# Optimization experiments

Measured on AMD Instinct MI355X. Metric: run time of the kernel, lower is better.

The kernel has to match this reference:

```python
import jax, jax.numpy as jnp
import numpy as np

N, E, G, S = 200000, 800000, 2048, 128
NUM_OPS, NUM_ETYPES, NUMERIC = 64, 4, 12
H, TEXT, VOCAB, OUT = 256, 64, 30000, 512
IN0 = 32 + NUMERIC  # 44


def _ln(h, eps=1e-5):
    # nn.LayerNorm with default (ones/zeros) affine, created fresh each forward
    m = h.mean(-1, keepdims=True)
    v = ((h - m) ** 2).mean(-1, keepdims=True)
    return (h - m) * jax.lax.rsqrt(v + eps)


def _leaky(v):
    return jnp.where(v > 0, v, 0.1 * v)  # LeakyReLU(0.1)


def setup_inputs() -> dict:
    key = jax.random.key(0)
    ks = jax.random.split(key, 40)
    x = jax.random.normal(ks[0], (N, 1 + NUMERIC), jnp.float32)
    x = x.at[:, 0].set(jax.random.randint(ks[1], (N,), 0, NUM_OPS).astype(jnp.float32))
    inp = {
        'x': x,
        'edge_index': jax.random.randint(ks[2], (2, E), 0, N),
        'edge_attr': jax.random.randint(ks[3], (E,), 0, NUM_ETYPES),
        'batch': jnp.sort(jax.random.randint(ks[4], (N,), 0, G)),
        'sql_ids': jax.random.randint(ks[5], (G, S), 0, VOCAB),
        'sql_mask': (jax.random.uniform(ks[6], (G, S)) > 0.3).astype(jnp.float32),
        'op_embed': jax.random.normal(ks[7], (NUM_OPS, 32), jnp.float32),
        'edge_embed': jax.random.normal(ks[8], (NUM_ETYPES, 16), jnp.float32),
        'token_embed': jax.random.normal(ks[9], (VOCAB, TEXT), jnp.float32).at[0].set(0.0),  # padding_idx=0
    }
    dims = [IN0, H, H]
    k = 10
    for i, d in enumerate(dims):
        inp[f'lin_w{i}'] = jax.random.normal(ks[k], (d, 16), jnp.float32) * 0.05; k += 1
        inp[f'lin_b{i}'] = jnp.zeros((d,), jnp.float32)
        inp[f'eps{i}'] = jnp.zeros((), jnp.float32)  # train_eps init 0
        inp[f'W1_{i}'] = jax.random.normal(ks[k], (H, d), jnp.float32) * 0.05; k += 1
        inp[f'b1_{i}'] = jnp.zeros((H,), jnp.float32)
        inp[f'W2_{i}'] = jax.random.normal(ks[k], (H, H), jnp.float32) * 0.05; k += 1
        inp[f'b2_{i}'] = jnp.zeros((H,), jnp.float32)
    inp['mW1'] = jax.random.normal(ks[k], (H, H + 3 + TEXT), jnp.float32) * 0.05; k += 1
    inp['mb1'] = jnp.zeros((H,), jnp.float32)
    inp['mW2'] = jax.random.normal(ks[k], (OUT, H), jnp.float32) * 0.05
    inp['mb2'] = jnp.zeros((OUT,), jnp.float32)
    return inp


def reference(x, edge_index, edge_attr, batch, sql_ids, sql_mask,
              op_embed, edge_embed, token_embed,
              lin_w0, lin_b0, eps0, W1_0, b1_0, W2_0, b2_0,
              lin_w1, lin_b1, eps1, W1_1, b1_1, W2_1, b2_1,
              lin_w2, lin_b2, eps2, W1_2, b1_2, W2_2, b2_2,
              mW1, mb1, mW2, mb2):
    op_ids = jnp.clip(x[:, 0].astype(jnp.int32), 0, NUM_OPS - 1)
    nums = x[:, 1:]
    e_idx = jnp.minimum(edge_attr, NUM_ETYPES - 1)  # clamp_max
    edge_emb = edge_embed[e_idx]                    # [E,16]
    h = jnp.concatenate([op_embed[op_ids], nums], 1)  # [N,44]
    src, dst = edge_index[0], edge_index[1]
    convs = [(lin_w0, lin_b0, eps0, W1_0, b1_0, W2_0, b2_0),
             (lin_w1, lin_b1, eps1, W1_1, b1_1, W2_1, b2_1),
             (lin_w2, lin_b2, eps2, W1_2, b1_2, W2_2, b2_2)]
    for (lw, lb, eps, W1, b1, W2, b2) in convs:
        h_in = h
        # GINEConv: msg = relu(x_j + Lin(edge_attr)); sum-aggregate at dst
        msg = jax.nn.relu(h[src] + edge_emb @ lw.T + lb)        # [E,d]
        aggr = jax.ops.segment_sum(msg, dst, num_segments=h.shape[0])
        z = (1.0 + eps) * h + aggr
        h = jax.nn.relu(z @ W1.T + b1) @ W2.T + b2              # conv MLP -> [N,H]
        h = _ln(h)
        h = _leaky(h + h_in) if h_in.shape[-1] == h.shape[-1] else _leaky(h)
    # graph pooling
    g = jax.ops.segment_sum(h, batch, num_segments=G)            # global_add_pool
    count = jax.ops.segment_sum(jnp.ones((h.shape[0],), h.dtype), batch, num_segments=G)
    denom = jnp.maximum(count, 1.0)                              # scatter_mean semantics
    fanout_mean = jax.ops.segment_sum(x[:, 5], batch, num_segments=G) / denom
    cost_mean = jax.ops.segment_sum(x[:, 4], batch, num_segments=G) / denom
    graph_sum = jnp.stack([count, fanout_mean, cost_mean], 1)    # [G,3]
    # text pooling (masked mean)
    emb = token_embed[sql_ids]                                   # [G,S,TEXT]
    summed = (emb * sql_mask[..., None]).sum(1)
    lengths = jnp.maximum(sql_mask.sum(1, keepdims=True), 1.0)
    text_feat = summed / lengths
    cat = jnp.concatenate([g, graph_sum, text_feat], 1)          # [G, H+3+TEXT]
    hid = _leaky(cat @ mW1.T + mb1)                              # Dropout(0.1) is identity in eval
    return hid @ mW2.T + mb2                                     # [G, OUT]
```

## Files before the change

kernel.cpp:

```cpp
#include <hip/hip_runtime.h>

#define NN 200000
#define EE 800000
#define GG 2048
#define NBLK ((NN + 255) / 256)

typedef __attribute__((ext_vector_type(8))) short short8;
typedef __attribute__((ext_vector_type(4))) float f32x4;

__device__ __forceinline__ float bf2f(ushort u){
  unsigned x = ((unsigned)u) << 16;
  return __uint_as_float(x);
}
__device__ __forceinline__ ushort f2bf(float f){
  unsigned x = __float_as_uint(f);
  x += 0x7fffu + ((x >> 16) & 1u);
  return (ushort)(x >> 16);
}

__device__ __forceinline__ void swz256(const float* __restrict__ W, ushort* __restrict__ o, int idx){
  int ks = idx >> 13, rem = idx & 8191;
  int j16 = rem >> 9, rem2 = rem & 511;
  int ln = rem2 >> 3, t = rem2 & 7;
  int row = j16*16 + (ln & 15);
  int k = ks*32 + (ln >> 4)*8 + t;
  o[idx] = f2bf(W[(size_t)row*256 + k]);
}

__global__ __launch_bounds__(256) void prep_k(
    const float* __restrict__ W10, const float* __restrict__ W20,
    const float* __restrict__ W11, const float* __restrict__ W21,
    const float* __restrict__ W12, const float* __restrict__ W22,
    const float* __restrict__ lw0, const float* __restrict__ lb0,
    const float* __restrict__ lw1, const float* __restrict__ lb1,
    const float* __restrict__ lw2, const float* __restrict__ lb2,
    const float* __restrict__ eE, const float* __restrict__ mW1,
    const float* __restrict__ mW2,
    ushort* __restrict__ wb10, ushort* __restrict__ wb20,
    ushort* __restrict__ wb11, ushort* __restrict__ wb21,
    ushort* __restrict__ wb12, ushort* __restrict__ wb22,
    ushort* __restrict__ mW1b, ushort* __restrict__ mW2b,
    float* __restrict__ eb)
{
  int b = blockIdx.x, tid = threadIdx.x;
  if (b < 64){
    int idx = b*256 + tid;
    int ks = idx >> 13, rem = idx & 8191;
    int j16 = rem >> 9, rem2 = rem & 511;
    int ln = rem2 >> 3, t = rem2 & 7;
    int row = j16*16 + (ln & 15);
    int k = ks*32 + (ln >> 4)*8 + t;
    wb10[idx] = (k < 44) ? f2bf(W10[row*44 + k]) : (ushort)0;
    return;
  }
  b -= 64;
  if (b < 256){ swz256(W20, wb20, b*256+tid); return; } b -= 256;
  if (b < 256){ swz256(W11, wb11, b*256+tid); return; } b -= 256;
  if (b < 256){ swz256(W21, wb21, b*256+tid); return; } b -= 256;
  if (b < 256){ swz256(W12, wb12, b*256+tid); return; } b -= 256;
  if (b < 256){ swz256(W22, wb22, b*256+tid); return; } b -= 256;
  if (b < 384){
    int idx = b*256 + tid; int o = idx / 384, k = idx - o*384;
    mW1b[idx] = (k < 323) ? f2bf(mW1[(size_t)o*323 + k]) : (ushort)0;
    return;
  }
  b -= 384;
  if (b < 512){ int idx = b*256+tid; mW2b[idx] = f2bf(mW2[idx]); return; } b -= 512;
  int li = b >> 2, t = b & 3;
  const float* lw = (li == 0) ? lw0 : ((li == 1) ? lw1 : lw2);
  const float* lb = (li == 0) ? lb0 : ((li == 1) ? lb1 : lb2);
  int d = (li == 0) ? 44 : 256;
  float v = 0.f;
  if (tid < d){
    float a = 0.f;
    #pragma unroll
    for (int j = 0; j < 16; j++) a += eE[t*16 + j] * lw[tid*16 + j];
    v = a + lb[tid];
  }
  eb[(li*4 + t)*256 + tid] = v;
}

__global__ __launch_bounds__(256) void build_h0_k(
    const float* __restrict__ x, const float* __restrict__ opE, ushort* __restrict__ h0)
{
  int idx = blockIdx.x*256 + threadIdx.x;
  int i = idx >> 6, c = idx & 63;
  float v = 0.f;
  if (c < 32){
    int op = (int)x[(size_t)i*13];
    op = op < 0 ? 0 : (op > 63 ? 63 : op);
    v = opE[op*32 + c];
  } else if (c < 44){
    v = x[(size_t)i*13 + (c - 31)];
  }
  h0[idx] = f2bf(v);
}

__global__ __launch_bounds__(256) void deg_k(const int* __restrict__ dst, int* __restrict__ D){
  int e = blockIdx.x*256 + threadIdx.x;
  atomicAdd(&D[dst[e]], 1);
}
__global__ __launch_bounds__(256) void scan1_k(int* __restrict__ D, int* __restrict__ bsum){
  __shared__ int s[256];
  int b = blockIdx.x, t = threadIdx.x, idx = b*256 + t;
  int v = (idx < NN) ? D[idx] : 0;
  s[t] = v; __syncthreads();
  for (int off = 1; off < 256; off <<= 1){
    int u = (t >= off) ? s[t-off] : 0;
    __syncthreads();
    s[t] += u;
    __syncthreads();
  }
  if (idx < NN) D[idx] = s[t] - v;
  if (t == 255) bsum[b] = s[255];
}
__global__ __launch_bounds__(256) void scan2_k(int* __restrict__ bsum){
  __shared__ int s[256];
  __shared__ int carry;
  int t = threadIdx.x;
  if (t == 0) carry = 0;
  __syncthreads();
  for (int c0 = 0; c0 < NBLK; c0 += 256){
    int idx = c0 + t;
    int v = (idx < NBLK) ? bsum[idx] : 0;
    s[t] = v; __syncthreads();
    for (int off = 1; off < 256; off <<= 1){
      int u = (t >= off) ? s[t-off] : 0;
      __syncthreads();
      s[t] += u;
      __syncthreads();
    }
    int ex = s[t] - v + carry;
    if (idx < NBLK) bsum[idx] = ex;
    int tot = s[255];
    __syncthreads();
    if (t == 0) carry += tot;
    __syncthreads();
  }
}
__global__ __launch_bounds__(256) void scan3_k(int* __restrict__ D, const int* __restrict__ bsum){
  int b = blockIdx.x, idx = b*256 + threadIdx.x;
  if (idx < NN) D[idx] += bsum[b];
}
__global__ __launch_bounds__(256) void fill_k(const int* __restrict__ src, const int* __restrict__ dst,
                                              const int* __restrict__ et, int* __restrict__ D,
                                              int* __restrict__ csr){
  int e = blockIdx.x*256 + threadIdx.x;
  int d = dst[e];
  int t = et[e]; t = t < 3 ? t : 3;
  int pos = atomicAdd(&D[d], 1);
  csr[pos] = src[e] | (t << 18);
}

template<int KD, int RESID>
__global__ __launch_bounds__(256) void layerf_k(
    const ushort* __restrict__ hsrc, const int* __restrict__ Dend, const int* __restrict__ csr,
    const float* __restrict__ ebL,
    const ushort* __restrict__ W1s, const float* __restrict__ b1,
    const ushort* __restrict__ W2s, const float* __restrict__ b2,
    const float* __restrict__ epsp, ushort* __restrict__ hout)
{
  __shared__ ushort ZT[32][264];
  __shared__ ushort HT[RESID ? 32 : 1][264];
  __shared__ float ebs[1024];
  __shared__ float red1[32][4], red2[32][4], mnL[32], rsL[32];
  const int tid = threadIdx.x, lane = tid & 63, wv = tid >> 6;
  const int l15 = lane & 15, lq = lane >> 4;
  const int rowBase = blockIdx.x * 32;
  const float epv = 1.0f + epsp[0];
  const char* hb = (const char*)hsrc;

  if (KD == 256){
    for (int i = tid; i < 1024; i += 256) ebs[i] = ebL[i];
  } else {
    if (tid < 256) ebs[tid] = ebL[(tid >> 6)*256 + (tid & 63)];
  }
  __syncthreads();

  if (KD == 256){
    int nz; asm("v_mov_b32 %0, 0" : "=v"(nz));
    const int c = lane * 4;
    const unsigned c2 = lane * 8;
    #pragma unroll 1
    for (int it = 0; it < 2; it++){
      int rr0 = wv*8 + it*4;
      int r0 = rowBase + rr0;
      float4 A0, A1, A2, A3;
      {
        ushort4 q0 = *(const ushort4*)(hb + (size_t)(r0+0)*512 + c2);
        ushort4 q1 = *(const ushort4*)(hb + (size_t)(r0+1)*512 + c2);
        ushort4 q2 = *(const ushort4*)(hb + (size_t)(r0+2)*512 + c2);
        ushort4 q3 = *(const ushort4*)(hb + (size_t)(r0+3)*512 + c2);
        if (RESID){
          *(ushort4*)&HT[rr0+0][c] = q0;
          *(ushort4*)&HT[rr0+1][c] = q1;
          *(ushort4*)&HT[rr0+2][c] = q2;
          *(ushort4*)&HT[rr0+3][c] = q3;
        }
        A0 = make_float4(epv*bf2f(q0.x), epv*bf2f(q0.y), epv*bf2f(q0.z), epv*bf2f(q0.w));
        A1 = make_float4(epv*bf2f(q1.x), epv*bf2f(q1.y), epv*bf2f(q1.z), epv*bf2f(q1.w));
        A2 = make_float4(epv*bf2f(q2.x), epv*bf2f(q2.y), epv*bf2f(q2.z), epv*bf2f(q2.w));
        A3 = make_float4(epv*bf2f(q3.x), epv*bf2f(q3.y), epv*bf2f(q3.z), epv*bf2f(q3.w));
      }
      int bm1 = (r0 == 0) ? 0 : Dend[r0-1];
      int e0 = Dend[r0], e1 = Dend[r0+1], e2 = Dend[r0+2], e3 = Dend[r0+3];
      int st0 = bm1, st1 = e0, st2 = e1, st3 = e2;
      int n0 = e0 - st0, n1 = e1 - st1, n2 = e2 - st2, n3 = e3 - st3;
      int nmax = n0 > n1 ? n0 : n1;
      nmax = nmax > n2 ? nmax : n2;
      nmax = nmax > n3 ? nmax : n3;
      ushort4 z4; z4.x = z4.y = z4.z = z4.w = 0;
      ushort4 sv0 = z4, sv1 = z4, sv2 = z4, sv3 = z4;
      int t0 = 0, t1 = 0, t2 = 0, t3 = 0;
      int q0 = 0, q1 = 0, q2 = 0, q3 = 0;
      if (n0 > 0){ int p = csr[st0 + nz]; sv0 = *(const ushort4*)(hb + (unsigned)((p & 0x3FFFF) << 9) + c2); t0 = ((p >> 18) & 3)*256; }
      if (n1 > 0){ int p = csr[st1 + nz]; sv1 = *(const ushort4*)(hb + (unsigned)((p & 0x3FFFF) << 9) + c2); t1 = ((p >> 18) & 3)*256; }
      if (n2 > 0){ int p = csr[st2 + nz]; sv2 = *(const ushort4*)(hb + (unsigned)((p & 0x3FFFF) << 9) + c2); t2 = ((p >> 18) & 3)*256; }
      if (n3 > 0){ int p = csr[st3 + nz]; sv3 = *(const ushort4*)(hb + (unsigned)((p & 0x3FFFF) << 9) + c2); t3 = ((p >> 18) & 3)*256; }
      if (n0 > 1) q0 = csr[st0 + 1 + nz];
      if (n1 > 1) q1 = csr[st1 + 1 + nz];
      if (n2 > 1) q2 = csr[st2 + 1 + nz];
      if (n3 > 1) q3 = csr[st3 + 1 + nz];
      for (int k = 0; k < nmax; k++){
        ushort4 c0 = sv0, c1 = sv1, c2v = sv2, c3 = sv3;
        int u0 = t0, u1 = t1, u2 = t2, u3 = t3;
        if (k+1 < n0){ int p = q0; sv0 = *(const ushort4*)(hb + (unsigned)((p & 0x3FFFF) << 9) + c2); t0 = ((p >> 18) & 3)*256; if (k+2 < n0) q0 = csr[st0 + k + 2 + nz]; }
        if (k+1 < n1){ int p = q1; sv1 = *(const ushort4*)(hb + (unsigned)((p & 0x3FFFF) << 9) + c2); t1 = ((p >> 18) & 3)*256; if (k+2 < n1) q1 = csr[st1 + k + 2 + nz]; }
        if (k+1 < n2){ int p = q2; sv2 = *(const ushort4*)(hb + (unsigned)((p & 0x3FFFF) << 9) + c2); t2 = ((p >> 18) & 3)*256; if (k+2 < n2) q2 = csr[st2 + k + 2 + nz]; }
        if (k+1 < n3){ int p = q3; sv3 = *(const ushort4*)(hb + (unsigned)((p & 0x3FFFF) << 9) + c2); t3 = ((p >> 18) & 3)*256; if (k+2 < n3) q3 = csr[st3 + k + 2 + nz]; }
        if (k < n0){
          const float4 ev = *(const float4*)&ebs[u0 + c];
          float v;
          v = bf2f(c0.x) + ev.x; A0.x += v > 0.f ? v : 0.f;
          v = bf2f(c0.y) + ev.y; A0.y += v > 0.f ? v : 0.f;
          v = bf2f(c0.z) + ev.z; A0.z += v > 0.f ? v : 0.f;
          v = bf2f(c0.w) + ev.w; A0.w += v > 0.f ? v : 0.f;
        }
        if (k < n1){
          const float4 ev = *(const float4*)&ebs[u1 + c];
          float v;
          v = bf2f(c1.x) + ev.x; A1.x += v > 0.f ? v : 0.f;
          v = bf2f(c1.y) + ev.y; A1.y += v > 0.f ? v : 0.f;
          v = bf2f(c1.z) + ev.z; A1.z += v > 0.f ? v : 0.f;
          v = bf2f(c1.w) + ev.w; A1.w += v > 0.f ? v : 0.f;
        }
        if (k < n2){
          const float4 ev = *(const float4*)&ebs[u2 + c];
          float v;
          v = bf2f(c2v.x) + ev.x; A2.x += v > 0.f ? v : 0.f;
          v = bf2f(c2v.y) + ev.y; A2.y += v > 0.f ? v : 0.f;
          v = bf2f(c2v.z) + ev.z; A2.z += v > 0.f ? v : 0.f;
          v = bf2f(c2v.w) + ev.w; A2.w += v > 0.f ? v : 0.f;
        }
        if (k < n3){
          const float4 ev = *(const float4*)&ebs[u3 + c];
          float v;
          v = bf2f(c3.x) + ev.x; A3.x += v > 0.f ? v : 0.f;
          v = bf2f(c3.y) + ev.y; A3.y += v > 0.f ? v : 0.f;
          v = bf2f(c3.z) + ev.z; A3.z += v > 0.f ? v : 0.f;
          v = bf2f(c3.w) + ev.w; A3.w += v > 0.f ? v : 0.f;
        }
      }
      ushort4 o;
      o.x = f2bf(A0.x); o.y = f2bf(A0.y); o.z = f2bf(A0.z); o.w = f2bf(A0.w);
      *(ushort4*)&ZT[rr0+0][c] = o;
      o.x = f2bf(A1.x); o.y = f2bf(A1.y); o.z = f2bf(A1.z); o.w = f2bf(A1.w);
      *(ushort4*)&ZT[rr0+1][c] = o;
      o.x = f2bf(A2.x); o.y = f2bf(A2.y); o.z = f2bf(A2.z); o.w = f2bf(A2.w);
      *(ushort4*)&ZT[rr0+2][c] = o;
      o.x = f2bf(A3.x); o.y = f2bf(A3.y); o.z = f2bf(A3.z); o.w = f2bf(A3.w);
      *(ushort4*)&ZT[rr0+3][c] = o;
    }
  } else {
    const int c = l15 * 4;
    const unsigned c2 = l15 * 8;
    const int rrA = wv*8 + lq, rrB = rrA + 4;
    const int rA = rowBase + rrA, rB = rowBase + rrB;
    float aA0, aA1, aA2, aA3, aB0, aB1, aB2, aB3;
    {
      ushort4 hv = *(const ushort4*)(hb + (size_t)rA*128 + c2);
      aA0 = epv*bf2f(hv.x); aA1 = epv*bf2f(hv.y); aA2 = epv*bf2f(hv.z); aA3 = epv*bf2f(hv.w);
      hv = *(const ushort4*)(hb + (size_t)rB*128 + c2);
      aB0 = epv*bf2f(hv.x); aB1 = epv*bf2f(hv.y); aB2 = epv*bf2f(hv.z); aB3 = epv*bf2f(hv.w);
    }
    int stA = (rA == 0) ? 0 : Dend[rA-1], enA = Dend[rA];
    int stB = Dend[rB-1], enB = Dend[rB];
    int nA = enA - stA, nB = enB - stB;
    int nmax = nA > nB ? nA : nB;
    ushort4 svA, svB; int ttA = 0, ttB = 0, pA = 0, pB = 0;
    svA.x = svA.y = svA.z = svA.w = 0; svB = svA;
    if (nA > 0){ int p = csr[stA]; svA = *(const ushort4*)(hb + (unsigned)((p & 0x3FFFF) << 7) + c2); ttA = ((p >> 18) & 3)*64; }
    if (nB > 0){ int p = csr[stB]; svB = *(const ushort4*)(hb + (unsigned)((p & 0x3FFFF) << 7) + c2); ttB = ((p >> 18) & 3)*64; }
    if (nA > 1) pA = csr[stA+1];
    if (nB > 1) pB = csr[stB+1];
    for (int k = 0; k < nmax; k++){
      if (k < nA){
        ushort4 cu = svA;
        const float4 ev = *(const float4*)&ebs[ttA + c];
        if (k+1 < nA){
          int p = pA;
          svA = *(const ushort4*)(hb + (unsigned)((p & 0x3FFFF) << 7) + c2);
          ttA = ((p >> 18) & 3)*64;
          if (k+2 < nA) pA = csr[stA+k+2];
        }
        float v;
        v = bf2f(cu.x) + ev.x; aA0 += v > 0.f ? v : 0.f;
        v = bf2f(cu.y) + ev.y; aA1 += v > 0.f ? v : 0.f;
        v = bf2f(cu.z) + ev.z; aA2 += v > 0.f ? v : 0.f;
        v = bf2f(cu.w) + ev.w; aA3 += v > 0.f ? v : 0.f;
      }
      if (k < nB){
        ushort4 cu = svB;
        const float4 ev = *(const float4*)&ebs[ttB + c];
        if (k+1 < nB){
          int p = pB;
          svB = *(const ushort4*)(hb + (unsigned)((p & 0x3FFFF) << 7) + c2);
          ttB = ((p >> 18) & 3)*64;
          if (k+2 < nB) pB = csr[stB+k+2];
        }
        float v;
        v = bf2f(cu.x) + ev.x; aB0 += v > 0.f ? v : 0.f;
        v = bf2f(cu.y) + ev.y; aB1 += v > 0.f ? v : 0.f;
        v = bf2f(cu.z) + ev.z; aB2 += v > 0.f ? v : 0.f;
        v = bf2f(cu.w) + ev.w; aB3 += v > 0.f ? v : 0.f;
      }
    }
    ushort4 o;
    o.x = f2bf(aA0); o.y = f2bf(aA1); o.z = f2bf(aA2); o.w = f2bf(aA3);
    *(ushort4*)&ZT[rrA][c] = o;
    o.x = f2bf(aB0); o.y = f2bf(aB1); o.z = f2bf(aB2); o.w = f2bf(aB3);
    *(ushort4*)&ZT[rrB][c] = o;
  }
  __syncthreads();

  f32x4 acc[2][4];
  #pragma unroll
  for (int i = 0; i < 2; i++)
    #pragma unroll
    for (int j = 0; j < 4; j++){ f32x4 z = {0.f,0.f,0.f,0.f}; acc[i][j] = z; }

  #pragma unroll
  for (int s = 0; s < KD/32; s++){
    short8 af[2], bfv[4];
    #pragma unroll
    for (int j = 0; j < 4; j++)
      bfv[j] = *(const short8*)(W1s + ((size_t)(s*16 + wv*4 + j)*64 + lane)*8);
    #pragma unroll
    for (int i = 0; i < 2; i++)
      af[i] = *(const short8*)&ZT[i*16 + l15][s*32 + lq*8];
    #pragma unroll
    for (int i = 0; i < 2; i++)
      #pragma unroll
      for (int j = 0; j < 4; j++)
        acc[i][j] = __builtin_amdgcn_mfma_f32_16x16x32_bf16(af[i], bfv[j], acc[i][j], 0, 0, 0);
  }
  __syncthreads();

  {
    float b1c[4];
    #pragma unroll
    for (int j = 0; j < 4; j++) b1c[j] = b1[wv*64 + j*16 + l15];
    #pragma unroll
    for (int i = 0; i < 2; i++)
      #pragma unroll
      for (int j = 0; j < 4; j++){
        int cc = wv*64 + j*16 + l15;
        #pragma unroll
        for (int rg = 0; rg < 4; rg++){
          int r = i*16 + (lq << 2) + rg;
          float v = acc[i][j][rg] + b1c[j];
          v = v > 0.f ? v : 0.f;
          ZT[r][cc] = f2bf(v);
        }
      }
  }
  __syncthreads();

  #pragma unroll
  for (int i = 0; i < 2; i++)
    #pragma unroll
    for (int j = 0; j < 4; j++){ f32x4 z = {0.f,0.f,0.f,0.f}; acc[i][j] = z; }

  #pragma unroll
  for (int s = 0; s < 8; s++){
    short8 af[2], bfv[4];
    #pragma unroll
    for (int j = 0; j < 4; j++)
      bfv[j] = *(const short8*)(W2s + ((size_t)(s*16 + wv*4 + j)*64 + lane)*8);
    #pragma unroll
    for (int i = 0; i < 2; i++)
      af[i] = *(const short8*)&ZT[i*16 + l15][s*32 + lq*8];
    #pragma unroll
    for (int i = 0; i < 2; i++)
      #pragma unroll
      for (int j = 0; j < 4; j++)
        acc[i][j] = __builtin_amdgcn_mfma_f32_16x16x32_bf16(af[i], bfv[j], acc[i][j], 0, 0, 0);
  }

  float b2c[4];
  #pragma unroll
  for (int j = 0; j < 4; j++) b2c[j] = b2[wv*64 + j*16 + l15];
  #pragma unroll
  for (int i = 0; i < 2; i++){
    #pragma unroll
    for (int rg = 0; rg < 4; rg++){
      float s1 = 0.f, s2 = 0.f;
      #pragma unroll
      for (int j = 0; j < 4; j++){
        float y = acc[i][j][rg] + b2c[j];
        s1 += y; s2 += y*y;
      }
      #pragma unroll
      for (int m = 1; m < 16; m <<= 1){
        s1 += __shfl_xor(s1, m, 64);
        s2 += __shfl_xor(s2, m, 64);
      }
      if (l15 == 0){
        int r = i*16 + (lq << 2) + rg;
        red1[r][wv] = s1; red2[r][wv] = s2;
      }
    }
  }
  __syncthreads();
  if (tid < 32){
    float s1 = red1[tid][0] + red1[tid][1] + red1[tid][2] + red1[tid][3];
    float s2 = red2[tid][0] + red2[tid][1] + red2[tid][2] + red2[tid][3];
    float mn = s1 * (1.f/256.f);
    float vr = s2 * (1.f/256.f) - mn*mn;
    mnL[tid] = mn;
    rsL[tid] = rsqrtf(vr + 1e-5f);
  }
  __syncthreads();
  #pragma unroll
  for (int i = 0; i < 2; i++){
    #pragma unroll
    for (int rg = 0; rg < 4; rg++){
      int r = i*16 + (lq << 2) + rg;
      float mn = mnL[r], rs = rsL[r];
      #pragma unroll
      for (int j = 0; j < 4; j++){
        int cc = wv*64 + j*16 + l15;
        float y = acc[i][j][rg] + b2c[j];
        float v = (y - mn) * rs;
        if (!RESID) v = v > 0.f ? v : 0.1f*v;
        ZT[r][cc] = f2bf(v);
      }
    }
  }
  __syncthreads();
  #pragma unroll
  for (int p = 0; p < 8; p++){
    int r = p*4 + (tid >> 6);
    int cs = (tid & 63) * 4;
    ushort4 zt = *(const ushort4*)&ZT[r][cs];
    ushort4 o;
    if (RESID){
      ushort4 rv = *(const ushort4*)&HT[r][cs];
      float v0 = bf2f(zt.x) + bf2f(rv.x);
      float v1 = bf2f(zt.y) + bf2f(rv.y);
      float v2 = bf2f(zt.z) + bf2f(rv.z);
      float v3 = bf2f(zt.w) + bf2f(rv.w);
      o.x = f2bf(v0 > 0.f ? v0 : 0.1f*v0);
      o.y = f2bf(v1 > 0.f ? v1 : 0.1f*v1);
      o.z = f2bf(v2 > 0.f ? v2 : 0.1f*v2);
      o.w = f2bf(v3 > 0.f ? v3 : 0.1f*v3);
    } else {
      o = zt;
    }
    *(ushort4*)(hout + (size_t)(rowBase + r)*256 + cs) = o;
  }
}

__global__ __launch_bounds__(256) void readout_k(
    const ushort* __restrict__ h, const int* __restrict__ batch, const float* __restrict__ x,
    const int* __restrict__ sqlIds, const float* __restrict__ sqlMask,
    const float* __restrict__ tok, ushort* __restrict__ catb)
{
  int g = blockIdx.x, tid = threadIdx.x;
  const int lane = tid & 63, wv = tid >> 6;
  __shared__ int se[2];
  __shared__ float part[4][256];
  __shared__ float tpart[4][64];
  __shared__ float mpart[4];
  __shared__ float xs[2];
  if (tid < 2){
    int target = g + tid;
    int lo = 0, hi = NN;
    while (lo < hi){ int mid = (lo + hi) >> 1; if (batch[mid] < target) lo = mid + 1; else hi = mid; }
    se[tid] = lo;
  }
  __syncthreads();
  int start = se[0], end = se[1];
  {
    float a0 = 0.f, a1 = 0.f, a2 = 0.f, a3 = 0.f;
    for (int i = start + wv; i < end; i += 4){
      ushort4 q = *(const ushort4*)(h + (size_t)i*256 + lane*4);
      a0 += bf2f(q.x); a1 += bf2f(q.y); a2 += bf2f(q.z); a3 += bf2f(q.w);
    }
    part[wv][lane*4 + 0] = a0;
    part[wv][lane*4 + 1] = a1;
    part[wv][lane*4 + 2] = a2;
    part[wv][lane*4 + 3] = a3;
  }
  if (wv >= 2){
    int col = (wv == 2) ? 5 : 4;
    float s = 0.f;
    for (int i = start + lane; i < end; i += 64) s += x[(size_t)i*13 + col];
    #pragma unroll
    for (int m = 1; m < 64; m <<= 1) s += __shfl_xor(s, m, 64);
    if (lane == 0) xs[wv - 2] = s;
  }
  {
    int c = lane;
    float acc = 0.f, m = 0.f;
    for (int s = wv; s < 128; s += 4){
      int id = sqlIds[g*128 + s];
      float mk = sqlMask[g*128 + s];
      m += mk;
      acc += tok[(size_t)id*64 + c] * mk;
    }
    tpart[wv][c] = acc;
    if (c == 0) mpart[wv] = m;
  }
  __syncthreads();
  {
    float gsum = part[0][tid] + part[1][tid] + part[2][tid] + part[3][tid];
    catb[(size_t)g*384 + tid] = f2bf(gsum);
  }
  if (tid == 0){
    float cnt = (float)(end - start);
    float dn = cnt > 1.f ? cnt : 1.f;
    catb[(size_t)g*384 + 256] = f2bf(cnt);
    catb[(size_t)g*384 + 257] = f2bf(xs[0] / dn);
    catb[(size_t)g*384 + 258] = f2bf(xs[1] / dn);
  }
  if (tid < 64){
    float L = mpart[0] + mpart[1] + mpart[2] + mpart[3];
    L = L > 1.f ? L : 1.f;
    float tsum = tpart[0][tid] + tpart[1][tid] + tpart[2][tid] + tpart[3][tid];
    catb[(size_t)g*384 + 259 + tid] = f2bf(tsum / L);
  }
  if (tid >= 64 && tid < 125){
    catb[(size_t)g*384 + 259 + tid] = 0;
  }
}

__global__ __launch_bounds__(256) void head1_k(
    const ushort* __restrict__ catb, const ushort* __restrict__ W1b,
    const float* __restrict__ b1, ushort* __restrict__ hidb)
{
  __shared__ ushort smem[64*72 + 256*72];
  ushort (*As)[72] = (ushort(*)[72])smem;
  ushort (*Ws)[72] = (ushort(*)[72])(smem + 64*72);
  const int tid = threadIdx.x, lane = tid & 63, wv = tid >> 6;
  const int rowBase = blockIdx.x * 64;
  f32x4 acc[4][4];
  #pragma unroll
  for (int i = 0; i < 4; i++)
    #pragma unroll
    for (int j = 0; j < 4; j++){ f32x4 z = {0.f,0.f,0.f,0.f}; acc[i][j] = z; }

  for (int k0 = 0; k0 < 384; k0 += 64){
    __syncthreads();
    #pragma unroll
    for (int p = 0; p < 4; p++){
      int r = p*16 + (tid >> 4);
      int kk = (tid & 15) * 4;
      *(ushort4*)&As[r][kk] = *(const ushort4*)(catb + (size_t)(rowBase + r)*384 + k0 + kk);
    }
    #pragma unroll
    for (int p = 0; p < 16; p++){
      int oc = p*16 + (tid >> 4);
      int kk = (tid & 15) * 4;
      *(ushort4*)&Ws[oc][kk] = *(const ushort4*)(W1b + (size_t)oc*384 + k0 + kk);
    }
    __syncthreads();
    #pragma unroll
    for (int kc = 0; kc < 2; kc++){
      short8 af[4], bfv[4];
      #pragma unroll
      for (int i = 0; i < 4; i++)
        af[i] = *(const short8*)&As[i*16 + (lane & 15)][kc*32 + (lane >> 4)*8];
      #pragma unroll
      for (int j = 0; j < 4; j++)
        bfv[j] = *(const short8*)&Ws[wv*64 + j*16 + (lane & 15)][kc*32 + (lane >> 4)*8];
      #pragma unroll
      for (int i = 0; i < 4; i++)
        #pragma unroll
        for (int j = 0; j < 4; j++)
          acc[i][j] = __builtin_amdgcn_mfma_f32_16x16x32_bf16(af[i], bfv[j], acc[i][j], 0, 0, 0);
    }
  }
  __syncthreads();
  ushort (*Cs)[264] = (ushort(*)[264])smem;
  #pragma unroll
  for (int j = 0; j < 4; j++){
    int cc = wv*64 + j*16 + (lane & 15);
    float bb = b1[cc];
    #pragma unroll
    for (int i = 0; i < 4; i++){
      #pragma unroll
      for (int rg = 0; rg < 4; rg++){
        int r = i*16 + ((lane >> 4) << 2) + rg;
        float v = acc[i][j][rg] + bb;
        v = v > 0.f ? v : 0.1f*v;
        Cs[r][cc] = f2bf(v);
      }
    }
  }
  __syncthreads();
  #pragma unroll
  for (int p = 0; p < 16; p++){
    int r = p*4 + (tid >> 6);
    int c = (tid & 63) * 4;
    *(ushort4*)(hidb + (size_t)(rowBase + r)*256 + c) = *(const ushort4*)&Cs[r][c];
  }
}

__global__ __launch_bounds__(256) void head2_k(
    const ushort* __restrict__ hidb, const ushort* __restrict__ W2b,
    const float* __restrict__ b2, float* __restrict__ out)
{
  __shared__ float smemf[128*132];
  ushort (*As)[72] = (ushort(*)[72])smemf;
  ushort (*Bs)[72] = (ushort(*)[72])((ushort*)smemf + 128*72);
  const int tid = threadIdx.x, lane = tid & 63, wv = tid >> 6;
  const int wr = (wv >> 1) * 64;
  const int wc = (wv & 1) * 64;
  const int rowBase = blockIdx.x * 128;
  const int colBase = blockIdx.y * 128;
  const int lr = tid >> 4, lk = (tid & 15) * 4;

  f32x4 acc[4][4];
  #pragma unroll
  for (int i = 0; i < 4; i++)
    #pragma unroll
    for (int j = 0; j < 4; j++){ f32x4 z = {0.f,0.f,0.f,0.f}; acc[i][j] = z; }

  for (int k0 = 0; k0 < 256; k0 += 64){
    __syncthreads();
    #pragma unroll
    for (int p = 0; p < 8; p++){
      int r = lr + p*16;
      *(ushort4*)&As[r][lk] = *(const ushort4*)(hidb + (size_t)(rowBase + r)*256 + k0 + lk);
      *(ushort4*)&Bs[r][lk] = *(const ushort4*)(W2b + (size_t)(colBase + r)*256 + k0 + lk);
    }
    __syncthreads();
    #pragma unroll
    for (int kc = 0; kc < 2; kc++){
      short8 af[4], bfv[4];
      #pragma unroll
      for (int i = 0; i < 4; i++)
        af[i] = *(const short8*)&As[wr + i*16 + (lane & 15)][kc*32 + (lane >> 4)*8];
      #pragma unroll
      for (int j = 0; j < 4; j++)
        bfv[j] = *(const short8*)&Bs[wc + j*16 + (lane & 15)][kc*32 + (lane >> 4)*8];
      #pragma unroll
      for (int i = 0; i < 4; i++)
        #pragma unroll
        for (int j = 0; j < 4; j++)
          acc[i][j] = __builtin_amdgcn_mfma_f32_16x16x32_bf16(af[i], bfv[j], acc[i][j], 0, 0, 0);
    }
  }
  __syncthreads();
  float (*Cs)[132] = (float(*)[132])smemf;
  #pragma unroll
  for (int j = 0; j < 4; j++){
    int cl = wc + j*16 + (lane & 15);
    float bb = b2[colBase + cl];
    #pragma unroll
    for (int i = 0; i < 4; i++){
      int r0 = wr + i*16 + ((lane >> 4) << 2);
      #pragma unroll
      for (int rg = 0; rg < 4; rg++)
        Cs[r0 + rg][cl] = acc[i][j][rg] + bb;
    }
  }
  __syncthreads();
  #pragma unroll
  for (int p = 0; p < 16; p++){
    int r = (tid >> 5) + p*8;
    int c4 = (tid & 31) * 4;
    *(float4*)(out + (size_t)(rowBase + r)*512 + colBase + c4) = *(const float4*)&Cs[r][c4];
  }
}

extern "C" void kernel_launch(void* const* d_in, const int* in_sizes, int n_in,
                              void* d_out, int out_size, void* d_ws, size_t ws_size,
                              hipStream_t stream)
{
  const float* x       = (const float*)d_in[0];
  const int*   ei      = (const int*)d_in[1];
  const int*   src     = ei;
  const int*   dst     = ei + EE;
  const int*   eattr   = (const int*)d_in[2];
  const int*   batch   = (const int*)d_in[3];
  const int*   sqlIds  = (const int*)d_in[4];
  const float* sqlMask = (const float*)d_in[5];
  const float* opE     = (const float*)d_in[6];
  const float* eE      = (const float*)d_in[7];
  const float* tok     = (const float*)d_in[8];
  const float* lw0 = (const float*)d_in[9],  *lb0 = (const float*)d_in[10], *eps0 = (const float*)d_in[11];
  const float* W10 = (const float*)d_in[12], *b10 = (const float*)d_in[13];
  const float* W20 = (const float*)d_in[14], *b20 = (const float*)d_in[15];
  const float* lw1 = (const float*)d_in[16], *lb1 = (const float*)d_in[17], *eps1 = (const float*)d_in[18];
  const float* W11 = (const float*)d_in[19], *b11 = (const float*)d_in[20];
  const float* W21 = (const float*)d_in[21], *b21 = (const float*)d_in[22];
  const float* lw2 = (const float*)d_in[23], *lb2 = (const float*)d_in[24], *eps2 = (const float*)d_in[25];
  const float* W12 = (const float*)d_in[26], *b12 = (const float*)d_in[27];
  const float* W22 = (const float*)d_in[28], *b22 = (const float*)d_in[29];
  const float* mW1 = (const float*)d_in[30], *mb1 = (const float*)d_in[31];
  const float* mW2 = (const float*)d_in[32], *mb2 = (const float*)d_in[33];
  float* out = (float*)d_out;

  char* ws = (char*)d_ws;
  size_t off = 0;
  const size_t NB256 = (size_t)NN*256*2;
  ushort* bufH    = (ushort*)(ws + off); off += NB256;
  char*   region  = ws + off;            off += NB256;
  ushort* h0      = (ushort*)region;
  ushort* hPong   = (ushort*)region;
  ushort* catb    = (ushort*)region;
  ushort* hidb    = (ushort*)(region + (size_t)GG*384*2);
  ushort* wb10 = (ushort*)(ws + off); off += (size_t)256*64*2;
  ushort* wb20 = (ushort*)(ws + off); off += (size_t)65536*2;
  ushort* wb11 = (ushort*)(ws + off); off += (size_t)65536*2;
  ushort* wb21 = (ushort*)(ws + off); off += (size_t)65536*2;
  ushort* wb12 = (ushort*)(ws + off); off += (size_t)65536*2;
  ushort* wb22 = (ushort*)(ws + off); off += (size_t)65536*2;
  ushort* mW1b = (ushort*)(ws + off); off += (size_t)256*384*2;
  ushort* mW2b = (ushort*)(ws + off); off += (size_t)512*256*2;
  float*  eb   = (float*)(ws + off);  off += (size_t)3*4*256*4;
  int* D    = (int*)(ws + off); off += (size_t)NN*4;
  int* bsum = (int*)(ws + off); off += (size_t)NBLK*4;
  int* csr  = (int*)(ws + off); off += (size_t)EE*4;
  size_t needFast = off;

  if (ws_size < needFast) return;

  prep_k<<<2252, 256, 0, stream>>>(W10, W20, W11, W21, W12, W22,
                                   lw0, lb0, lw1, lb1, lw2, lb2, eE, mW1, mW2,
                                   wb10, wb20, wb11, wb21, wb12, wb22, mW1b, mW2b, eb);
  build_h0_k<<<50000, 256, 0, stream>>>(x, opE, h0);

  hipMemsetAsync(D, 0, (size_t)NN*4, stream);
  deg_k<<<3125, 256, 0, stream>>>(dst, D);
  scan1_k<<<NBLK, 256, 0, stream>>>(D, bsum);
  scan2_k<<<1, 256, 0, stream>>>(bsum);
  scan3_k<<<NBLK, 256, 0, stream>>>(D, bsum);
  fill_k<<<3125, 256, 0, stream>>>(src, dst, eattr, D, csr);

  layerf_k<64,0><<<6250, 256, 0, stream>>>(h0,    D, csr, eb,        wb10, b10, wb20, b20, eps0, bufH);
  layerf_k<256,1><<<6250, 256, 0, stream>>>(bufH, D, csr, eb + 1024, wb11, b11, wb21, b21, eps1, hPong);
  layerf_k<256,1><<<6250, 256, 0, stream>>>(hPong,D, csr, eb + 2048, wb12, b12, wb22, b22, eps2, bufH);

  readout_k<<<GG, 256, 0, stream>>>(bufH, batch, x, sqlIds, sqlMask, tok, catb);
  head1_k<<<32, 256, 0, stream>>>(catb, mW1b, mb1, hidb);
  head2_k<<<dim3(16, 4), 256, 0, stream>>>(hidb, mW2b, mb2, out);
}
```

Measured before the change: 832.8 us.

## Gather neighbor features from int8 per-row-quantized shadow copies in GIN layers

Layers 0 and 1 now also write an 8-bit per-row-scaled copy of their output plus a per-row scale. Layers 1 and 2 read that int8 copy in the edge-gather aggregation instead of bf16 rows, which halves the bytes fetched per neighbor. The bf16 output is still written for the residual path and readout. The shadow path runs only when the workspace is large enough. This adds extra writes, a wave-wide max reduction per row and quantization error in the aggregation.

```diff
diff --git a/kernel.cpp b/kernel.cpp
--- a/kernel.cpp
+++ b/kernel.cpp
@@ -152,13 +152,15 @@
   csr[pos] = src[e] | (t << 18);
 }
 
-template<int KD, int RESID>
+template<int KD, int RESID, int WRS, int RDS>
 __global__ __launch_bounds__(256) void layerf_k(
     const ushort* __restrict__ hsrc, const int* __restrict__ Dend, const int* __restrict__ csr,
     const float* __restrict__ ebL,
     const ushort* __restrict__ W1s, const float* __restrict__ b1,
     const ushort* __restrict__ W2s, const float* __restrict__ b2,
-    const float* __restrict__ epsp, ushort* __restrict__ hout)
+    const float* __restrict__ epsp, ushort* __restrict__ hout,
+    const unsigned char* __restrict__ q8in, const float* __restrict__ sclin,
+    unsigned char* __restrict__ q8out, float* __restrict__ sclout)
 {
   __shared__ ushort ZT[32][264];
   __shared__ ushort HT[RESID ? 32 : 1][264];
@@ -181,6 +183,7 @@
     int nz; asm("v_mov_b32 %0, 0" : "=v"(nz));
     const int c = lane * 4;
     const unsigned c2 = lane * 8;
+    const unsigned c1 = lane * 4;
     #pragma unroll 1
     for (int it = 0; it < 2; it++){
       int rr0 = wv*8 + it*4;
@@ -209,56 +212,113 @@
       int nmax = n0 > n1 ? n0 : n1;
       nmax = nmax > n2 ? nmax : n2;
       nmax = nmax > n3 ? nmax : n3;
-      ushort4 z4; z4.x = z4.y = z4.z = z4.w = 0;
-      ushort4 sv0 = z4, sv1 = z4, sv2 = z4, sv3 = z4;
-      int t0 = 0, t1 = 0, t2 = 0, t3 = 0;
-      int q0 = 0, q1 = 0, q2 = 0, q3 = 0;
-      if (n0 > 0){ int p = csr[st0 + nz]; sv0 = *(const ushort4*)(hb + (unsigned)((p & 0x3FFFF) << 9) + c2); t0 = ((p >> 18) & 3)*256; }
-      if (n1 > 0){ int p = csr[st1 + nz]; sv1 = *(const ushort4*)(hb + (unsigned)((p & 0x3FFFF) << 9) + c2); t1 = ((p >> 18) & 3)*256; }
-      if (n2 > 0){ int p = csr[st2 + nz]; sv2 = *(const ushort4*)(hb + (unsigned)((p & 0x3FFFF) << 9) + c2); t2 = ((p >> 18) & 3)*256; }
-      if (n3 > 0){ int p = csr[st3 + nz]; sv3 = *(const ushort4*)(hb + (unsigned)((p & 0x3FFFF) << 9) + c2); t3 = ((p >> 18) & 3)*256; }
-      if (n0 > 1) q0 = csr[st0 + 1 + nz];
-      if (n1 > 1) q1 = csr[st1 + 1 + nz];
-      if (n2 > 1) q2 = csr[st2 + 1 + nz];
-      if (n3 > 1) q3 = csr[st3 + 1 + nz];
-      for (int k = 0; k < nmax; k++){
-        ushort4 c0 = sv0, c1 = sv1, c2v = sv2, c3 = sv3;
-        int u0 = t0, u1 = t1, u2 = t2, u3 = t3;
-        if (k+1 < n0){ int p = q0; sv0 = *(const ushort4*)(hb + (unsigned)((p & 0x3FFFF) << 9) + c2); t0 = ((p >> 18) & 3)*256; if (k+2 < n0) q0 = csr[st0 + k + 2 + nz]; }
-        if (k+1 < n1){ int p = q1; sv1 = *(const ushort4*)(hb + (unsigned)((p & 0x3FFFF) << 9) + c2); t1 = ((p >> 18) & 3)*256; if (k+2 < n1) q1 = csr[st1 + k + 2 + nz]; }
-        if (k+1 < n2){ int p = q2; sv2 = *(const ushort4*)(hb + (unsigned)((p & 0x3FFFF) << 9) + c2); t2 = ((p >> 18) & 3)*256; if (k+2 < n2) q2 = csr[st2 + k + 2 + nz]; }
-        if (k+1 < n3){ int p = q3; sv3 = *(const ushort4*)(hb + (unsigned)((p & 0x3FFFF) << 9) + c2); t3 = ((p >> 18) & 3)*256; if (k+2 < n3) q3 = csr[st3 + k + 2 + nz]; }
-        if (k < n0){
-          const float4 ev = *(const float4*)&ebs[u0 + c];
-          float v;
-          v = bf2f(c0.x) + ev.x; A0.x += v > 0.f ? v : 0.f;
-          v = bf2f(c0.y) + ev.y; A0.y += v > 0.f ? v : 0.f;
-          v = bf2f(c0.z) + ev.z; A0.z += v > 0.f ? v : 0.f;
-          v = bf2f(c0.w) + ev.w; A0.w += v > 0.f ? v : 0.f;
+
+      if (RDS){
+        unsigned sv0 = 0, sv1 = 0, sv2 = 0, sv3 = 0;
+        float ss0 = 0.f, ss1 = 0.f, ss2 = 0.f, ss3 = 0.f;
+        int t0 = 0, t1 = 0, t2 = 0, t3 = 0;
+        int q0 = 0, q1 = 0, q2 = 0, q3 = 0;
+        if (n0 > 0){ int p = csr[st0 + nz]; unsigned rw = (unsigned)(p & 0x3FFFF); sv0 = *(const unsigned*)(q8in + ((size_t)rw<<8) + c1); ss0 = sclin[rw]; t0 = ((p >> 18) & 3)*256; }
+        if (n1 > 0){ int p = csr[st1 + nz]; unsigned rw = (unsigned)(p & 0x3FFFF); sv1 = *(const unsigned*)(q8in + ((size_t)rw<<8) + c1); ss1 = sclin[rw]; t1 = ((p >> 18) & 3)*256; }
+        if (n2 > 0){ int p = csr[st2 + nz]; unsigned rw = (unsigned)(p & 0x3FFFF); sv2 = *(const unsigned*)(q8in + ((size_t)rw<<8) + c1); ss2 = sclin[rw]; t2 = ((p >> 18) & 3)*256; }
+        if (n3 > 0){ int p = csr[st3 + nz]; unsigned rw = (unsigned)(p & 0x3FFFF); sv3 = *(const unsigned*)(q8in + ((size_t)rw<<8) + c1); ss3 = sclin[rw]; t3 = ((p >> 18) & 3)*256; }
+        if (n0 > 1) q0 = csr[st0 + 1 + nz];
+        if (n1 > 1) q1 = csr[st1 + 1 + nz];
+        if (n2 > 1) q2 = csr[st2 + 1 + nz];
+        if (n3 > 1) q3 = csr[st3 + 1 + nz];
+        for (int k = 0; k < nmax; k++){
+          unsigned c0 = sv0, c1v = sv1, c2v = sv2, c3v = sv3;
+          float d0 = ss0, d1 = ss1, d2 = ss2, d3 = ss3;
+          int u0 = t0, u1 = t1, u2 = t2, u3 = t3;
+          if (k+1 < n0){ int p = q0; unsigned rw = (unsigned)(p & 0x3FFFF); sv0 = *(const unsigned*)(q8in + ((size_t)rw<<8) + c1); ss0 = sclin[rw]; t0 = ((p >> 18) & 3)*256; if (k+2 < n0) q0 = csr[st0 + k + 2 + nz]; }
+          if (k+1 < n1){ int p = q1; unsigned rw = (unsigned)(p & 0x3FFFF); sv1 = *(const unsigned*)(q8in + ((size_t)rw<<8) + c1); ss1 = sclin[rw]; t1 = ((p >> 18) & 3)*256; if (k+2 < n1) q1 = csr[st1 + k + 2 + nz]; }
+          if (k+1 < n2){ int p = q2; unsigned rw = (unsigned)(p & 0x3FFFF); sv2 = *(const unsigned*)(q8in + ((size_t)rw<<8) + c1); ss2 = sclin[rw]; t2 = ((p >> 18) & 3)*256; if (k+2 < n2) q2 = csr[st2 + k + 2 + nz]; }
+          if (k+1 < n3){ int p = q3; unsigned rw = (unsigned)(p & 0x3FFFF); sv3 = *(const unsigned*)(q8in + ((size_t)rw<<8) + c1); ss3 = sclin[rw]; t3 = ((p >> 18) & 3)*256; if (k+2 < n3) q3 = csr[st3 + k + 2 + nz]; }
+          if (k < n0){
+            const float4 ev = *(const float4*)&ebs[u0 + c];
+            float o = d0 * -128.f, v;
+            v = fmaf((float)(c0 & 0xffu),        d0, o) + ev.x; A0.x += v > 0.f ? v : 0.f;
+            v = fmaf((float)((c0 >> 8) & 0xffu), d0, o) + ev.y; A0.y += v > 0.f ? v : 0.f;
+            v = fmaf((float)((c0 >> 16) & 0xffu),d0, o) + ev.z; A0.z += v > 0.f ? v : 0.f;
+            v = fmaf((float)(c0 >> 24),          d0, o) + ev.w; A0.w += v > 0.f ? v : 0.f;
+          }
+          if (k < n1){
+            const float4 ev = *(const float4*)&ebs[u1 + c];
+            float o = d1 * -128.f, v;
+            v = fmaf((float)(c1v & 0xffu),        d1, o) + ev.x; A1.x += v > 0.f ? v : 0.f;
+            v = fmaf((float)((c1v >> 8) & 0xffu), d1, o) + ev.y; A1.y += v > 0.f ? v : 0.f;
+            v = fmaf((float)((c1v >> 16) & 0xffu),d1, o) + ev.z; A1.z += v > 0.f ? v : 0.f;
+            v = fmaf((float)(c1v >> 24),          d1, o) + ev.w; A1.w += v > 0.f ? v : 0.f;
+          }
+          if (k < n2){
+            const float4 ev = *(const float4*)&ebs[u2 + c];
+            float o = d2 * -128.f, v;
+            v = fmaf((float)(c2v & 0xffu),        d2, o) + ev.x; A2.x += v > 0.f ? v : 0.f;
+            v = fmaf((float)((c2v >> 8) & 0xffu), d2, o) + ev.y; A2.y += v > 0.f ? v : 0.f;
+            v = fmaf((float)((c2v >> 16) & 0xffu),d2, o) + ev.z; A2.z += v > 0.f ? v : 0.f;
+            v = fmaf((float)(c2v >> 24),          d2, o) + ev.w; A2.w += v > 0.f ? v : 0.f;
+          }
+          if (k < n3){
+            const float4 ev = *(const float4*)&ebs[u3 + c];
+            float o = d3 * -128.f, v;
+            v = fmaf((float)(c3v & 0xffu),        d3, o) + ev.x; A3.x += v > 0.f ? v : 0.f;
+            v = fmaf((float)((c3v >> 8) & 0xffu), d3, o) + ev.y; A3.y += v > 0.f ? v : 0.f;
+            v = fmaf((float)((c3v >> 16) & 0xffu),d3, o) + ev.z; A3.z += v > 0.f ? v : 0.f;
+            v = fmaf((float)(c3v >> 24),          d3, o) + ev.w; A3.w += v > 0.f ? v : 0.f;
+          }
         }
-        if (k < n1){
-          const float4 ev = *(const float4*)&ebs[u1 + c];
-          float v;
-          v = bf2f(c1.x) + ev.x; A1.x += v > 0.f ? v : 0.f;
-          v = bf2f(c1.y) + ev.y; A1.y += v > 0.f ? v : 0.f;
-          v = bf2f(c1.z) + ev.z; A1.z += v > 0.f ? v : 0.f;
-          v = bf2f(c1.w) + ev.w; A1.w += v > 0.f ? v : 0.f;
-        }
-        if (k < n2){
-          const float4 ev = *(const float4*)&ebs[u2 + c];
-          float v;
-          v = bf2f(c2v.x) + ev.x; A2.x += v > 0.f ? v : 0.f;
-          v = bf2f(c2v.y) + ev.y; A2.y += v > 0.f ? v : 0.f;
-          v = bf2f(c2v.z) + ev.z; A2.z += v > 0.f ? v : 0.f;
-          v = bf2f(c2v.w) + ev.w; A2.w += v > 0.f ? v : 0.f;
-        }
-        if (k < n3){
-          const float4 ev = *(const float4*)&ebs[u3 + c];
-          float v;
-          v = bf2f(c3.x) + ev.x; A3.x += v > 0.f ? v : 0.f;
-          v = bf2f(c3.y) + ev.y; A3.y += v > 0.f ? v : 0.f;
-          v = bf2f(c3.z) + ev.z; A3.z += v > 0.f ? v : 0.f;
-          v = bf2f(c3.w) + ev.w; A3.w += v > 0.f ? v : 0.f;
+      } else {
+        ushort4 z4; z4.x = z4.y = z4.z = z4.w = 0;
+        ushort4 sv0 = z4, sv1 = z4, sv2 = z4, sv3 = z4;
+        int t0 = 0, t1 = 0, t2 = 0, t3 = 0;
+        int q0 = 0, q1 = 0, q2 = 0, q3 = 0;
+        if (n0 > 0){ int p = csr[st0 + nz]; sv0 = *(const ushort4*)(hb + (unsigned)((p & 0x3FFFF) << 9) + c2); t0 = ((p >> 18) & 3)*256; }
+        if (n1 > 0){ int p = csr[st1 + nz]; sv1 = *(const ushort4*)(hb + (unsigned)((p & 0x3FFFF) << 9) + c2); t1 = ((p >> 18) & 3)*256; }
+        if (n2 > 0){ int p = csr[st2 + nz]; sv2 = *(const ushort4*)(hb + (unsigned)((p & 0x3FFFF) << 9) + c2); t2 = ((p >> 18) & 3)*256; }
+        if (n3 > 0){ int p = csr[st3 + nz]; sv3 = *(const ushort4*)(hb + (unsigned)((p & 0x3FFFF) << 9) + c2); t3 = ((p >> 18) & 3)*256; }
+        if (n0 > 1) q0 = csr[st0 + 1 + nz];
+        if (n1 > 1) q1 = csr[st1 + 1 + nz];
+        if (n2 > 1) q2 = csr[st2 + 1 + nz];
+        if (n3 > 1) q3 = csr[st3 + 1 + nz];
+        for (int k = 0; k < nmax; k++){
+          ushort4 c0 = sv0, c1v = sv1, c2v = sv2, c3v = sv3;
+          int u0 = t0, u1 = t1, u2 = t2, u3 = t3;
+          if (k+1 < n0){ int p = q0; sv0 = *(const ushort4*)(hb + (unsigned)((p & 0x3FFFF) << 9) + c2); t0 = ((p >> 18) & 3)*256; if (k+2 < n0) q0 = csr[st0 + k + 2 + nz]; }
+          if (k+1 < n1){ int p = q1; sv1 = *(const ushort4*)(hb + (unsigned)((p & 0x3FFFF) << 9) + c2); t1 = ((p >> 18) & 3)*256; if (k+2 < n1) q1 = csr[st1 + k + 2 + nz]; }
+          if (k+1 < n2){ int p = q2; sv2 = *(const ushort4*)(hb + (unsigned)((p & 0x3FFFF) << 9) + c2); t2 = ((p >> 18) & 3)*256; if (k+2 < n2) q2 = csr[st2 + k + 2 + nz]; }
+          if (k+1 < n3){ int p = q3; sv3 = *(const ushort4*)(hb + (unsigned)((p & 0x3FFFF) << 9) + c2); t3 = ((p >> 18) & 3)*256; if (k+2 < n3) q3 = csr[st3 + k + 2 + nz]; }
+          if (k < n0){
+            const float4 ev = *(const float4*)&ebs[u0 + c];
+            float v;
+            v = bf2f(c0.x) + ev.x; A0.x += v > 0.f ? v : 0.f;
+            v = bf2f(c0.y) + ev.y; A0.y += v > 0.f ? v : 0.f;
+            v = bf2f(c0.z) + ev.z; A0.z += v > 0.f ? v : 0.f;
+            v = bf2f(c0.w) + ev.w; A0.w += v > 0.f ? v : 0.f;
+          }
+          if (k < n1){
+            const float4 ev = *(const float4*)&ebs[u1 + c];
+            float v;
+            v = bf2f(c1v.x) + ev.x; A1.x += v > 0.f ? v : 0.f;
+            v = bf2f(c1v.y) + ev.y; A1.y += v > 0.f ? v : 0.f;
+            v = bf2f(c1v.z) + ev.z; A1.z += v > 0.f ? v : 0.f;
+            v = bf2f(c1v.w) + ev.w; A1.w += v > 0.f ? v : 0.f;
+          }
+          if (k < n2){
+            const float4 ev = *(const float4*)&ebs[u2 + c];
+            float v;
+            v = bf2f(c2v.x) + ev.x; A2.x += v > 0.f ? v : 0.f;
+            v = bf2f(c2v.y) + ev.y; A2.y += v > 0.f ? v : 0.f;
+            v = bf2f(c2v.z) + ev.z; A2.z += v > 0.f ? v : 0.f;
+            v = bf2f(c2v.w) + ev.w; A2.w += v > 0.f ? v : 0.f;
+          }
+          if (k < n3){
+            const float4 ev = *(const float4*)&ebs[u3 + c];
+            float v;
+            v = bf2f(c3v.x) + ev.x; A3.x += v > 0.f ? v : 0.f;
+            v = bf2f(c3v.y) + ev.y; A3.y += v > 0.f ? v : 0.f;
+            v = bf2f(c3v.z) + ev.z; A3.z += v > 0.f ? v : 0.f;
+            v = bf2f(c3v.w) + ev.w; A3.w += v > 0.f ? v : 0.f;
+          }
         }
       }
       ushort4 o;
@@ -453,21 +513,42 @@
     int r = p*4 + (tid >> 6);
     int cs = (tid & 63) * 4;
     ushort4 zt = *(const ushort4*)&ZT[r][cs];
+    float v0, v1, v2, v3;
     ushort4 o;
     if (RESID){
       ushort4 rv = *(const ushort4*)&HT[r][cs];
-      float v0 = bf2f(zt.x) + bf2f(rv.x);
-      float v1 = bf2f(zt.y) + bf2f(rv.y);
-      float v2 = bf2f(zt.z) + bf2f(rv.z);
-      float v3 = bf2f(zt.w) + bf2f(rv.w);
-      o.x = f2bf(v0 > 0.f ? v0 : 0.1f*v0);
-      o.y = f2bf(v1 > 0.f ? v1 : 0.1f*v1);
-      o.z = f2bf(v2 > 0.f ? v2 : 0.1f*v2);
-      o.w = f2bf(v3 > 0.f ? v3 : 0.1f*v3);
+      v0 = bf2f(zt.x) + bf2f(rv.x);
+      v1 = bf2f(zt.y) + bf2f(rv.y);
+      v2 = bf2f(zt.z) + bf2f(rv.z);
+      v3 = bf2f(zt.w) + bf2f(rv.w);
+      v0 = v0 > 0.f ? v0 : 0.1f*v0;
+      v1 = v1 > 0.f ? v1 : 0.1f*v1;
+      v2 = v2 > 0.f ? v2 : 0.1f*v2;
+      v3 = v3 > 0.f ? v3 : 0.1f*v3;
+      o.x = f2bf(v0); o.y = f2bf(v1); o.z = f2bf(v2); o.w = f2bf(v3);
     } else {
       o = zt;
+      v0 = bf2f(zt.x); v1 = bf2f(zt.y); v2 = bf2f(zt.z); v3 = bf2f(zt.w);
     }
     *(ushort4*)(hout + (size_t)(rowBase + r)*256 + cs) = o;
+    if (WRS){
+      float m = fmaxf(fmaxf(fabsf(v0), fabsf(v1)), fmaxf(fabsf(v2), fabsf(v3)));
+      #pragma unroll
+      for (int k = 1; k < 64; k <<= 1) m = fmaxf(m, __shfl_xor(m, k, 64));
+      float inv = m > 0.f ? 127.f/m : 0.f;
+      int grow = rowBase + r;
+      if ((tid & 63) == 0) sclout[grow] = m * (1.f/127.f);
+      int q0 = __float2int_rn(fmaf(v0, inv, 128.f));
+      int q1 = __float2int_rn(fmaf(v1, inv, 128.f));
+      int q2 = __float2int_rn(fmaf(v2, inv, 128.f));
+      int q3 = __float2int_rn(fmaf(v3, inv, 128.f));
+      q0 = q0 < 0 ? 0 : (q0 > 255 ? 255 : q0);
+      q1 = q1 < 0 ? 0 : (q1 > 255 ? 255 : q1);
+      q2 = q2 < 0 ? 0 : (q2 > 255 ? 255 : q2);
+      q3 = q3 < 0 ? 0 : (q3 > 255 ? 255 : q3);
+      unsigned dw = (unsigned)q0 | ((unsigned)q1 << 8) | ((unsigned)q2 << 16) | ((unsigned)q3 << 24);
+      *(unsigned*)(q8out + (size_t)grow*256 + cs) = dw;
+    }
   }
 }
 
@@ -736,7 +817,14 @@
   int* csr  = (int*)(ws + off); off += (size_t)EE*4;
   size_t needFast = off;
 
+  unsigned char* q8A = (unsigned char*)(ws + off); off += (size_t)NN*256;
+  float* sclA = (float*)(ws + off); off += (size_t)NN*4;
+  unsigned char* q8B = (unsigned char*)(ws + off); off += (size_t)NN*256;
+  float* sclB = (float*)(ws + off); off += (size_t)NN*4;
+  size_t needShadow = off;
+
   if (ws_size < needFast) return;
+  const bool useShad = (ws_size >= needShadow);
 
   prep_k<<<2252, 256, 0, stream>>>(W10, W20, W11, W21, W12, W22,
                                    lw0, lb0, lw1, lb1, lw2, lb2, eE, mW1, mW2,
@@ -750,9 +838,21 @@
   scan3_k<<<NBLK, 256, 0, stream>>>(D, bsum);
   fill_k<<<3125, 256, 0, stream>>>(src, dst, eattr, D, csr);
 
-  layerf_k<64,0><<<6250, 256, 0, stream>>>(h0,    D, csr, eb,        wb10, b10, wb20, b20, eps0, bufH);
-  layerf_k<256,1><<<6250, 256, 0, stream>>>(bufH, D, csr, eb + 1024, wb11, b11, wb21, b21, eps1, hPong);
-  layerf_k<256,1><<<6250, 256, 0, stream>>>(hPong,D, csr, eb + 2048, wb12, b12, wb22, b22, eps2, bufH);
+  if (useShad){
+    layerf_k<64,0,1,0><<<6250, 256, 0, stream>>>(h0,    D, csr, eb,        wb10, b10, wb20, b20, eps0, bufH,
+                                                 nullptr, nullptr, q8A, sclA);
+    layerf_k<256,1,1,1><<<6250, 256, 0, stream>>>(bufH, D, csr, eb + 1024, wb11, b11, wb21, b21, eps1, hPong,
+                                                 q8A, sclA, q8B, sclB);
+    layerf_k<256,1,0,1><<<6250, 256, 0, stream>>>(hPong,D, csr, eb + 2048, wb12, b12, wb22, b22, eps2, bufH,
+                                                 q8B, sclB, nullptr, nullptr);
+  } else {
+    layerf_k<64,0,0,0><<<6250, 256, 0, stream>>>(h0,    D, csr, eb,        wb10, b10, wb20, b20, eps0, bufH,
+                                                 nullptr, nullptr, nullptr, nullptr);
+    layerf_k<256,1,0,0><<<6250, 256, 0, stream>>>(bufH, D, csr, eb + 1024, wb11, b11, wb21, b21, eps1, hPong,
+                                                 nullptr, nullptr, nullptr, nullptr);
+    layerf_k<256,1,0,0><<<6250, 256, 0, stream>>>(hPong,D, csr, eb + 2048, wb12, b12, wb22, b22, eps2, bufH,
+                                                 nullptr, nullptr, nullptr, nullptr);
+  }
 
   readout_k<<<GG, 256, 0, stream>>>(bufH, batch, x, sqlIds, sqlMask, tok, catb);
   head1_k<<<32, 256, 0, stream>>>(catb, mW1b, mb1, hidb);
```

Result: no change. 828.0 us (-0.6%).
